# Optimization experiments

Hardware: AMD Instinct MI355X
Metric: run time of the kernel (lower is better)

## Reference

```python
import jax, jax.numpy as jnp
import numpy as np

DIM = 384
H = 6
D = DIM // H
MLP = 4 * DIM
SCALE = D ** -0.5
LN_EPS = 1e-5


def _ln(x, w, b):
    m = jnp.mean(x, axis=-1, keepdims=True)
    v = jnp.mean((x - m) ** 2, axis=-1, keepdims=True)
    return (x - m) * jax.lax.rsqrt(v + LN_EPS) * w + b


def setup_inputs() -> dict:
    key = jax.random.key(0)
    ks = jax.random.split(key, 8)
    B, N = 8, 1024
    x = jax.random.normal(ks[0], (B, N, DIM), dtype=jnp.float32)
    # torch nn.Linear weights are [out, in]
    qkv_w = jax.random.normal(ks[1], (3 * DIM, DIM), dtype=jnp.float32) * (DIM ** -0.5)
    proj_w = jax.random.normal(ks[2], (DIM, DIM), dtype=jnp.float32) * (DIM ** -0.5)
    proj_b = jnp.zeros((DIM,), jnp.float32)
    # L2Q params, 'quadratic' init
    alpha = jnp.full((H, 1, 1), 0.125, jnp.float32)
    beta = jnp.full((H, 1, 1), 0.5, jnp.float32)
    gamma = jnp.zeros((H, 1, 1), jnp.float32)
    ln1_w = jnp.ones((DIM,), jnp.float32)
    ln1_b = jnp.zeros((DIM,), jnp.float32)
    ln2_w = jnp.ones((DIM,), jnp.float32)
    ln2_b = jnp.zeros((DIM,), jnp.float32)
    w1 = jax.random.normal(ks[3], (MLP, DIM), dtype=jnp.float32) * (DIM ** -0.5)
    b1 = jnp.zeros((MLP,), jnp.float32)
    w2 = jax.random.normal(ks[4], (DIM, MLP), dtype=jnp.float32) * (MLP ** -0.5)
    b2 = jnp.zeros((DIM,), jnp.float32)
    return {"x": x, "qkv_w": qkv_w, "proj_w": proj_w, "proj_b": proj_b,
            "alpha": alpha, "beta": beta, "gamma": gamma,
            "ln1_w": ln1_w, "ln1_b": ln1_b, "ln2_w": ln2_w, "ln2_b": ln2_b,
            "w1": w1, "b1": b1, "w2": w2, "b2": b2}


def reference(x, qkv_w, proj_w, proj_b, alpha, beta, gamma,
              ln1_w, ln1_b, ln2_w, ln2_b, w1, b1, w2, b2):
    B, N, C = x.shape
    # --- L2Q attention on LN(x) ---
    h = _ln(x, ln1_w, ln1_b)
    qkv = (h @ qkv_w.T).reshape(B, N, 3, H, D)
    q = qkv[:, :, 0].transpose(0, 2, 1, 3)  # [B,H,N,D]
    k = qkv[:, :, 1].transpose(0, 2, 1, 3)
    v = qkv[:, :, 2].transpose(0, 2, 1, 3)
    logits = jnp.einsum('bhnd,bhmd->bhnm', q, k) * SCALE
    attn = jax.nn.relu(alpha * logits ** 2 + beta * logits + gamma)
    attn = attn / (jnp.sum(attn, axis=-1, keepdims=True) + 1e-6)
    out = jnp.einsum('bhnm,bhmd->bhnd', attn, v)
    out = out.transpose(0, 2, 1, 3).reshape(B, N, C)
    x = x + out @ proj_w.T + proj_b
    # --- MLP on LN(x), exact GELU (torch default) ---
    h2 = _ln(x, ln2_w, ln2_b)
    m = jax.nn.gelu(h2 @ w1.T + b1, approximate=False)
    x = x + m @ w2.T + b2
    return x
```

## Files before the change

kernel.cpp:

```cpp
#include <hip/hip_runtime.h>
#include <hip/hip_bf16.h>
#include <math.h>

#define DIMC 384
#define NH 6
#define HD 64
#define MLPD 1536
#define BS 8
#define SEQ 1024
#define T_TOK (BS*SEQ)
#define TC ((size_t)T_TOK*DIMC)
#define QK_SCALE 0.125f

typedef __bf16 bf16;
typedef bf16 bf16x4 __attribute__((ext_vector_type(4)));
typedef bf16 bf16x8 __attribute__((ext_vector_type(8)));
typedef float floatx4 __attribute__((ext_vector_type(4)));

__device__ __forceinline__ void async_cp16(const void* gsrc, void* ldst) {
    __builtin_amdgcn_global_load_lds(
        (const __attribute__((address_space(1))) unsigned int*)gsrc,
        (__attribute__((address_space(3))) unsigned int*)ldst,
        16, 0, 0);
}

__global__ __launch_bounds__(256)
void cvt_all(const float* __restrict__ s0, const float* __restrict__ s1,
             const float* __restrict__ s2, const float* __restrict__ s3,
             bf16* __restrict__ dst) {
    int i = blockIdx.x * 256 + threadIdx.x;
    const int n0 = 110592, n1 = 36864, n2 = 147456;
    const float4* src; int j;
    if (i < n0)           { src = (const float4*)s0; j = i; }
    else if (i < n0+n1)   { src = (const float4*)s1; j = i - n0; }
    else if (i < n0+n1+n2){ src = (const float4*)s2; j = i - n0 - n1; }
    else                  { src = (const float4*)s3; j = i - n0 - n1 - n2; }
    float4 v = src[j];
    bf16x4 o; o[0] = (bf16)v.x; o[1] = (bf16)v.y; o[2] = (bf16)v.z; o[3] = (bf16)v.w;
    ((bf16x4*)dst)[i] = o;
}

__global__ __launch_bounds__(256)
void ln_kernel(const float* __restrict__ x, const float* __restrict__ w,
               const float* __restrict__ b, bf16* __restrict__ out) {
    int row = blockIdx.x * 4 + (threadIdx.x >> 6);
    int t = threadIdx.x & 63;
    const float* xr = x + (size_t)row * DIMC;
    float vals[6];
    float s = 0.f;
    #pragma unroll
    for (int i = 0; i < 6; i++) { vals[i] = xr[t + i*64]; s += vals[i]; }
    #pragma unroll
    for (int m = 32; m; m >>= 1) s += __shfl_xor(s, m);
    float mean = s * (1.0f / DIMC);
    float sq = 0.f;
    #pragma unroll
    for (int i = 0; i < 6; i++) { float d = vals[i] - mean; sq += d * d; }
    #pragma unroll
    for (int m = 32; m; m >>= 1) sq += __shfl_xor(sq, m);
    float rstd = rsqrtf(sq * (1.0f / DIMC) + 1e-5f);
    bf16* orow = out + (size_t)row * DIMC;
    #pragma unroll
    for (int i = 0; i < 6; i++) {
        int c = t + i*64;
        orow[c] = (bf16)((vals[i] - mean) * rstd * w[c] + b[c]);
    }
}

__global__ __launch_bounds__(256)
void ln2_fused(const float* __restrict__ x, const bf16* __restrict__ p0,
               const bf16* __restrict__ p1, const float* __restrict__ pb,
               const float* __restrict__ w, const float* __restrict__ b,
               float* __restrict__ x1, bf16* __restrict__ h) {
    int row = blockIdx.x * 4 + (threadIdx.x >> 6);
    int t = threadIdx.x & 63;
    size_t base = (size_t)row * DIMC;
    float vals[6];
    float s = 0.f;
    #pragma unroll
    for (int i = 0; i < 6; i++) {
        int c = t + i*64;
        float v = x[base + c] + (float)p0[base + c] + (float)p1[base + c] + pb[c];
        vals[i] = v; s += v;
    }
    #pragma unroll
    for (int m = 32; m; m >>= 1) s += __shfl_xor(s, m);
    float mean = s * (1.0f / DIMC);
    float sq = 0.f;
    #pragma unroll
    for (int i = 0; i < 6; i++) { float d = vals[i] - mean; sq += d * d; }
    #pragma unroll
    for (int m = 32; m; m >>= 1) sq += __shfl_xor(sq, m);
    float rstd = rsqrtf(sq * (1.0f / DIMC) + 1e-5f);
    #pragma unroll
    for (int i = 0; i < 6; i++) {
        int c = t + i*64;
        x1[base + c] = vals[i];
        h[base + c] = (bf16)((vals[i] - mean) * rstd * w[c] + b[c]);
    }
}

__global__ __launch_bounds__(256)
void reduce4(float* __restrict__ xo, const bf16* __restrict__ p0, const bf16* __restrict__ p1,
             const bf16* __restrict__ p2, const bf16* __restrict__ p3,
             const float* __restrict__ b2) {
    int i = blockIdx.x * 256 + threadIdx.x;
    float4 v = ((const float4*)xo)[i];
    int c = (i % 96) * 4;
    float4 bb = *(const float4*)(b2 + c);
    bf16x4 a0 = ((const bf16x4*)p0)[i], a1 = ((const bf16x4*)p1)[i];
    bf16x4 a2 = ((const bf16x4*)p2)[i], a3 = ((const bf16x4*)p3)[i];
    v.x += bb.x + (float)a0[0] + (float)a1[0] + (float)a2[0] + (float)a3[0];
    v.y += bb.y + (float)a0[1] + (float)a1[1] + (float)a2[1] + (float)a3[1];
    v.z += bb.z + (float)a0[2] + (float)a1[2] + (float)a2[2] + (float)a3[2];
    v.w += bb.w + (float)a0[3] + (float)a1[3] + (float)a2[3] + (float)a3[3];
    ((float4*)xo)[i] = v;
}

enum { EPI_NONE = 0, EPI_QKV = 1, EPI_GELU = 3 };

template<int EPI, int K, int KS, typename OutT>
__global__ __launch_bounds__(256)
void gemm_bt(const bf16* __restrict__ A, const bf16* __restrict__ W,
             const float* __restrict__ bias, OutT* out, int M, int N) {
    __shared__ __align__(16) bf16 Ash[128*32];
    __shared__ __align__(16) bf16 Bsh[128*32];
    constexpr int KB = K / KS;
    int tid = threadIdx.x;
    int lane = tid & 63, w = tid >> 6;
    int quad = lane >> 4, l16 = lane & 15;
    int rbase = blockIdx.y * 128 + (w >> 1) * 64;
    int cbase = blockIdx.x * 128 + (w & 1) * 64;
    int kbase = blockIdx.z * KB;
    int c1 = w * 64 + lane;
    int c2 = c1 + 256;
    const bf16* Ag1 = A + (size_t)(blockIdx.y*128 + (c1 >> 2)) * K + kbase + (c1 & 3) * 8;
    const bf16* Ag2 = A + (size_t)(blockIdx.y*128 + (c2 >> 2)) * K + kbase + (c2 & 3) * 8;
    const bf16* Wg1 = W + (size_t)(blockIdx.x*128 + (c1 >> 2)) * K + kbase + (c1 & 3) * 8;
    const bf16* Wg2 = W + (size_t)(blockIdx.x*128 + (c2 >> 2)) * K + kbase + (c2 & 3) * 8;
    bf16* As1 = Ash + c1 * 8;  bf16* As2 = Ash + c2 * 8;
    bf16* Bs1 = Bsh + c1 * 8;  bf16* Bs2 = Bsh + c2 * 8;

    int arow = (w >> 1) * 64;
    int brow = (w & 1) * 64;
    floatx4 acc[4][4] = {};
    #pragma unroll
    for (int kk = 0; kk < KB / 32; kk++) {
        __syncthreads();
        async_cp16(Ag1 + kk*32, As1);
        async_cp16(Ag2 + kk*32, As2);
        async_cp16(Wg1 + kk*32, Bs1);
        async_cp16(Wg2 + kk*32, Bs2);
        __syncthreads();
        bf16x8 a[4], bfr[4];
        #pragma unroll
        for (int tm = 0; tm < 4; tm++)
            a[tm] = *(const bf16x8*)&Ash[(arow + tm*16 + l16) * 32 + quad*8];
        #pragma unroll
        for (int tn = 0; tn < 4; tn++)
            bfr[tn] = *(const bf16x8*)&Bsh[(brow + tn*16 + l16) * 32 + quad*8];
        #pragma unroll
        for (int tm = 0; tm < 4; tm++)
            #pragma unroll
            for (int tn = 0; tn < 4; tn++)
                acc[tm][tn] = __builtin_amdgcn_mfma_f32_16x16x32_bf16(a[tm], bfr[tn], acc[tm][tn], 0, 0, 0);
    }

    #pragma unroll
    for (int tm = 0; tm < 4; tm++)
        #pragma unroll
        for (int tn = 0; tn < 4; tn++) {
            if constexpr (EPI == EPI_QKV) {
                int colb = cbase + tn*16 + l16;
                int which = colb / 384;
                int rowb = rbase + tm*16 + quad*4;
                int bb = rowb >> 10;
                if (which == 2) {
                    int rem = colb - 768;
                    int hh = rem >> 6, d = rem & 63;
                    int n = rowb & 1023;
                    bf16x4 pk;
                    #pragma unroll
                    for (int r = 0; r < 4; r++) pk[r] = (bf16)acc[tm][tn][r];
                    *(bf16x4*)((bf16*)out + 2*TC + (((size_t)(bb*NH + hh) * HD + d) << 10) + n) = pk;
                } else {
                    int rem = colb - which*384;
                    int hh = rem >> 6, d = rem & 63;
                    #pragma unroll
                    for (int r = 0; r < 4; r++) {
                        int n = (rowb & 1023) + r;
                        ((bf16*)out)[(size_t)which*TC + (((size_t)(bb*NH + hh) * SEQ + n) << 6) + d]
                            = (bf16)acc[tm][tn][r];
                    }
                }
            } else if constexpr (EPI == EPI_NONE) {
                OutT* ob = out + (size_t)blockIdx.z * M * N;
                #pragma unroll
                for (int r = 0; r < 4; r++) {
                    int row = rbase + tm*16 + quad*4 + r;
                    int col = cbase + tn*16 + l16;
                    ob[(size_t)row * N + col] = (OutT)acc[tm][tn][r];
                }
            } else {
                #pragma unroll
                for (int r = 0; r < 4; r++) {
                    int row = rbase + tm*16 + quad*4 + r;
                    int col = cbase + tn*16 + l16;
                    float v = acc[tm][tn][r] + bias[col];
                    v = 0.5f * v * (1.0f + erff(v * 0.70710678118f));
                    out[(size_t)row * N + col] = (OutT)v;
                }
            }
        }
}

__global__ __launch_bounds__(256)
void attn_kernel(const bf16* __restrict__ q, const bf16* __restrict__ k,
                 const bf16* __restrict__ vt, const float* __restrict__ alpha,
                 const float* __restrict__ beta, const float* __restrict__ gamma,
                 bf16* __restrict__ attn_out) {
    __shared__ __align__(16) char smem[36864];
    bf16  (*Psh)[72] = (bf16(*)[72])smem;
    float (*RedA)[68] = (float(*)[68])smem;
    float (*RedB)[68] = RedA + 64;

    int L = blockIdx.x;
    int xcd = L & 7, slot = L >> 3;
    int qt = slot & 15;
    int bh = xcd + ((slot >> 4) << 3);
    int bb = bh / NH, h = bh % NH;
    int q0 = qt * 64;
    int tid = threadIdx.x;
    int w = tid >> 6, lane = tid & 63, quad = lane >> 4, l16 = lane & 15;
    float av = alpha[h] * (QK_SCALE * QK_SCALE), bv = beta[h] * QK_SCALE, gv = gamma[h];
    const bf16* qb  = q  + (size_t)bh * SEQ * HD;
    const bf16* kb  = k  + (size_t)bh * SEQ * HD;
    const bf16* vtb = vt + (size_t)bh * HD * SEQ;

    bf16x8 qa[4][2];
    #pragma unroll
    for (int tm = 0; tm < 4; tm++)
        #pragma unroll
        for (int ks = 0; ks < 2; ks++)
            qa[tm][ks] = *(const bf16x8*)(qb + (size_t)(q0 + tm*16 + l16) * HD + ks*32 + quad*8);

    bf16x8 vone;
    #pragma unroll
    for (int j = 0; j < 8; j++) vone[j] = (bf16)1.0f;

    floatx4 o[4][4] = {};
    floatx4 rsacc[4] = {};
    int prow = w * 64;
    int rd_sw = ((l16 >> 2) & 3) << 3;
    int kt_base = w * 4;

    bf16x8 kf[2][4], kn[2][4], vf[2][4];
    #pragma unroll
    for (int ks = 0; ks < 2; ks++)
        #pragma unroll
        for (int tn = 0; tn < 4; tn++)
            kf[ks][tn] = *(const bf16x8*)(kb + (size_t)(kt_base*64 + tn*16 + l16) * HD + ks*32 + quad*8);

    #pragma unroll
    for (int t = 0; t < 4; t++) {
        int kb0 = (kt_base + t) * 64;
        if (t < 3) {
            int nb0 = kb0 + 64;
            #pragma unroll
            for (int ks = 0; ks < 2; ks++)
                #pragma unroll
                for (int tn = 0; tn < 4; tn++)
                    kn[ks][tn] = *(const bf16x8*)(kb + (size_t)(nb0 + tn*16 + l16) * HD + ks*32 + quad*8);
        }
        #pragma unroll
        for (int ks = 0; ks < 2; ks++)
            #pragma unroll
            for (int tn = 0; tn < 4; tn++)
                vf[ks][tn] = *(const bf16x8*)(vtb + (size_t)(tn*16 + l16) * SEQ + kb0 + ks*32 + quad*8);
        #pragma unroll
        for (int tm = 0; tm < 4; tm++) {
            floatx4 s[4] = {};
            #pragma unroll
            for (int ks = 0; ks < 2; ks++)
                #pragma unroll
                for (int tn = 0; tn < 4; tn++)
                    s[tn] = __builtin_amdgcn_mfma_f32_16x16x32_bf16(qa[tm][ks], kf[ks][tn], s[tn], 0, 0, 0);
            #pragma unroll
            for (int tn = 0; tn < 4; tn++)
                #pragma unroll
                for (int r = 0; r < 4; r++) {
                    float xx = s[tn][r];
                    float p = fmaxf((av*xx + bv)*xx + gv, 0.f);
                    int row = tm*16 + quad*4 + r;
                    int col = (tn*16 + l16) ^ (quad << 3);
                    Psh[prow + row][col] = (bf16)p;
                }
        }
        #pragma unroll
        for (int ks = 0; ks < 2; ks++) {
            bf16x8 pf[4];
            #pragma unroll
            for (int tm = 0; tm < 4; tm++)
                pf[tm] = *(const bf16x8*)&Psh[prow + tm*16 + l16][(ks*32 + quad*8) ^ rd_sw];
            #pragma unroll
            for (int tm = 0; tm < 4; tm++)
                rsacc[tm] = __builtin_amdgcn_mfma_f32_16x16x32_bf16(pf[tm], vone, rsacc[tm], 0, 0, 0);
            #pragma unroll
            for (int tm = 0; tm < 4; tm++)
                #pragma unroll
                for (int tn = 0; tn < 4; tn++)
                    o[tm][tn] = __builtin_amdgcn_mfma_f32_16x16x32_bf16(pf[tm], vf[ks][tn], o[tm][tn], 0, 0, 0);
        }
        if (t < 3) {
            #pragma unroll
            for (int ks = 0; ks < 2; ks++)
                #pragma unroll
                for (int tn = 0; tn < 4; tn++)
                    kf[ks][tn] = kn[ks][tn];
        }
    }

    __syncthreads();
    if (w & 1) {
        float (*R)[68] = (w == 1) ? RedA : RedB;
        #pragma unroll
        for (int tm = 0; tm < 4; tm++) {
            #pragma unroll
            for (int tn = 0; tn < 4; tn++)
                #pragma unroll
                for (int r = 0; r < 4; r++)
                    R[tm*16 + quad*4 + r][tn*16 + l16] = o[tm][tn][r];
            if (l16 == 0)
                #pragma unroll
                for (int r = 0; r < 4; r++)
                    R[tm*16 + quad*4 + r][64] = rsacc[tm][r];
        }
    }
    __syncthreads();
    if (!(w & 1)) {
        float (*R)[68] = (w == 0) ? RedA : RedB;
        #pragma unroll
        for (int tm = 0; tm < 4; tm++) {
            #pragma unroll
            for (int tn = 0; tn < 4; tn++)
                #pragma unroll
                for (int r = 0; r < 4; r++)
                    o[tm][tn][r] += R[tm*16 + quad*4 + r][tn*16 + l16];
            #pragma unroll
            for (int r = 0; r < 4; r++)
                rsacc[tm][r] += R[tm*16 + quad*4 + r][64];
        }
    }
    __syncthreads();
    if (w == 2) {
        #pragma unroll
        for (int tm = 0; tm < 2; tm++) {
            #pragma unroll
            for (int tn = 0; tn < 4; tn++)
                #pragma unroll
                for (int r = 0; r < 4; r++)
                    RedA[tm*16 + quad*4 + r][tn*16 + l16] = o[tm][tn][r];
            if (l16 == 0)
                #pragma unroll
                for (int r = 0; r < 4; r++)
                    RedA[tm*16 + quad*4 + r][64] = rsacc[tm][r];
        }
    } else if (w == 0) {
        #pragma unroll
        for (int tm = 2; tm < 4; tm++) {
            #pragma unroll
            for (int tn = 0; tn < 4; tn++)
                #pragma unroll
                for (int r = 0; r < 4; r++)
                    RedA[tm*16 + quad*4 + r][tn*16 + l16] = o[tm][tn][r];
            if (l16 == 0)
                #pragma unroll
                for (int r = 0; r < 4; r++)
                    RedA[tm*16 + quad*4 + r][64] = rsacc[tm][r];
        }
    }
    __syncthreads();
    if (w == 0) {
        #pragma unroll
        for (int tm = 0; tm < 2; tm++) {
            #pragma unroll
            for (int r = 0; r < 4; r++)
                rsacc[tm][r] += RedA[tm*16 + quad*4 + r][64];
            #pragma unroll
            for (int tn = 0; tn < 4; tn++)
                #pragma unroll
                for (int r = 0; r < 4; r++) {
                    float ov = o[tm][tn][r] + RedA[tm*16 + quad*4 + r][tn*16 + l16];
                    int n = q0 + tm*16 + quad*4 + r;
                    attn_out[((size_t)(bb*SEQ + n)) * DIMC + h*HD + tn*16 + l16] =
                        (bf16)(ov / (rsacc[tm][r] + 1e-6f));
                }
        }
    } else if (w == 2) {
        #pragma unroll
        for (int tm = 2; tm < 4; tm++) {
            #pragma unroll
            for (int r = 0; r < 4; r++)
                rsacc[tm][r] += RedA[tm*16 + quad*4 + r][64];
            #pragma unroll
            for (int tn = 0; tn < 4; tn++)
                #pragma unroll
                for (int r = 0; r < 4; r++) {
                    float ov = o[tm][tn][r] + RedA[tm*16 + quad*4 + r][tn*16 + l16];
                    int n = q0 + tm*16 + quad*4 + r;
                    attn_out[((size_t)(bb*SEQ + n)) * DIMC + h*HD + tn*16 + l16] =
                        (bf16)(ov / (rsacc[tm][r] + 1e-6f));
                }
        }
    }
}

extern "C" void kernel_launch(void* const* d_in, const int* in_sizes, int n_in,
                              void* d_out, int out_size, void* d_ws, size_t ws_size,
                              hipStream_t stream) {
    const float* x      = (const float*)d_in[0];
    const float* qkv_w  = (const float*)d_in[1];
    const float* proj_w = (const float*)d_in[2];
    const float* proj_b = (const float*)d_in[3];
    const float* alpha  = (const float*)d_in[4];
    const float* beta   = (const float*)d_in[5];
    const float* gamma  = (const float*)d_in[6];
    const float* ln1_w  = (const float*)d_in[7];
    const float* ln1_b  = (const float*)d_in[8];
    const float* ln2_w  = (const float*)d_in[9];
    const float* ln2_b  = (const float*)d_in[10];
    const float* w1     = (const float*)d_in[11];
    const float* b1     = (const float*)d_in[12];
    const float* w2     = (const float*)d_in[13];
    const float* b2     = (const float*)d_in[14];
    float* out = (float*)d_out;

    char* base = (char*)d_ws;
    bf16* wq_bf = (bf16*)base;
    bf16* wp_bf = wq_bf + 442368;
    bf16* w1_bf = wq_bf + 589824;
    bf16* w2_bf = wq_bf + 1179648;
    bf16* h      = (bf16*)(base + 3538944);
    bf16* qkv    = (bf16*)(base + 9830400);
    bf16* attn_o = (bf16*)(base + 28704768);
    bf16* m      = qkv;
    bf16* Pp     = (bf16*)(base + 34996224);
    bf16* Pm     = (bf16*)(base + 34996224);

    cvt_all<<<1728, 256, 0, stream>>>(qkv_w, proj_w, w1, w2, wq_bf);
    ln_kernel<<<T_TOK/4, 256, 0, stream>>>(x, ln1_w, ln1_b, h);
    gemm_bt<EPI_QKV, 384, 1, bf16><<<dim3(9, 64, 1), 256, 0, stream>>>(
        h, wq_bf, nullptr, qkv, T_TOK, 1152);
    attn_kernel<<<768, 256, 0, stream>>>(
        qkv, qkv + TC, qkv + 2*TC, alpha, beta, gamma, attn_o);
    gemm_bt<EPI_NONE, 384, 2, bf16><<<dim3(3, 64, 2), 256, 0, stream>>>(
        attn_o, wp_bf, nullptr, Pp, T_TOK, DIMC);
    ln2_fused<<<T_TOK/4, 256, 0, stream>>>(x, Pp, Pp + TC, proj_b, ln2_w, ln2_b, out, h);
    gemm_bt<EPI_GELU, 384, 1, bf16><<<dim3(12, 64, 1), 256, 0, stream>>>(
        h, w1_bf, b1, m, T_TOK, MLPD);
    gemm_bt<EPI_NONE, 1536, 4, bf16><<<dim3(3, 64, 4), 256, 0, stream>>>(
        m, w2_bf, nullptr, Pm, T_TOK, DIMC);
    reduce4<<<TC/4/256, 256, 0, stream>>>(out, Pm, Pm + TC, Pm + 2*TC, Pm + 3*TC, b2);
}
```

Baseline: 233.2 us.

## Halve attention query tile to 32 rows and double grid for occupancy

The attention kernel now processes 32 query rows per block instead of 64. The grid doubles to 1536 blocks, shared memory halves, and launch bounds request 4 blocks per CU. The K prefetch double-buffer is dropped: the next K tile is loaded straight into kf after QK^T, and V loads move after the P write, cutting register pressure. This trades per-block K/V reuse (each K/V tile is reloaded by twice as many blocks) for more waves in flight to hide latency.

```diff
diff --git a/kernel.cpp b/kernel.cpp
--- a/kernel.cpp
+++ b/kernel.cpp
@@ -214,22 +214,22 @@
         }
 }
 
-__global__ __launch_bounds__(256)
+__global__ __launch_bounds__(256, 4)
 void attn_kernel(const bf16* __restrict__ q, const bf16* __restrict__ k,
                  const bf16* __restrict__ vt, const float* __restrict__ alpha,
                  const float* __restrict__ beta, const float* __restrict__ gamma,
                  bf16* __restrict__ attn_out) {
-    __shared__ __align__(16) char smem[36864];
+    __shared__ __align__(16) char smem[18432];
     bf16  (*Psh)[72] = (bf16(*)[72])smem;
     float (*RedA)[68] = (float(*)[68])smem;
-    float (*RedB)[68] = RedA + 64;
+    float (*RedB)[68] = RedA + 32;
 
     int L = blockIdx.x;
     int xcd = L & 7, slot = L >> 3;
-    int qt = slot & 15;
-    int bh = xcd + ((slot >> 4) << 3);
+    int qt = slot & 31;
+    int bh = xcd + ((slot >> 5) << 3);
     int bb = bh / NH, h = bh % NH;
-    int q0 = qt * 64;
+    int q0 = qt * 32;
     int tid = threadIdx.x;
     int w = tid >> 6, lane = tid & 63, quad = lane >> 4, l16 = lane & 15;
     float av = alpha[h] * (QK_SCALE * QK_SCALE), bv = beta[h] * QK_SCALE, gv = gamma[h];
@@ -237,9 +237,9 @@
     const bf16* kb  = k  + (size_t)bh * SEQ * HD;
     const bf16* vtb = vt + (size_t)bh * HD * SEQ;
 
-    bf16x8 qa[4][2];
-    #pragma unroll
-    for (int tm = 0; tm < 4; tm++)
+    bf16x8 qa[2][2];
+    #pragma unroll
+    for (int tm = 0; tm < 2; tm++)
         #pragma unroll
         for (int ks = 0; ks < 2; ks++)
             qa[tm][ks] = *(const bf16x8*)(qb + (size_t)(q0 + tm*16 + l16) * HD + ks*32 + quad*8);
@@ -248,13 +248,13 @@
     #pragma unroll
     for (int j = 0; j < 8; j++) vone[j] = (bf16)1.0f;
 
-    floatx4 o[4][4] = {};
-    floatx4 rsacc[4] = {};
-    int prow = w * 64;
+    floatx4 o[2][4] = {};
+    floatx4 rsacc[2] = {};
+    int prow = w * 32;
     int rd_sw = ((l16 >> 2) & 3) << 3;
     int kt_base = w * 4;
 
-    bf16x8 kf[2][4], kn[2][4], vf[2][4];
+    bf16x8 kf[2][4], vf[2][4];
     #pragma unroll
     for (int ks = 0; ks < 2; ks++)
         #pragma unroll
@@ -264,21 +264,8 @@
     #pragma unroll
     for (int t = 0; t < 4; t++) {
         int kb0 = (kt_base + t) * 64;
-        if (t < 3) {
-            int nb0 = kb0 + 64;
-            #pragma unroll
-            for (int ks = 0; ks < 2; ks++)
-                #pragma unroll
-                for (int tn = 0; tn < 4; tn++)
-                    kn[ks][tn] = *(const bf16x8*)(kb + (size_t)(nb0 + tn*16 + l16) * HD + ks*32 + quad*8);
-        }
-        #pragma unroll
-        for (int ks = 0; ks < 2; ks++)
-            #pragma unroll
-            for (int tn = 0; tn < 4; tn++)
-                vf[ks][tn] = *(const bf16x8*)(vtb + (size_t)(tn*16 + l16) * SEQ + kb0 + ks*32 + quad*8);
-        #pragma unroll
-        for (int tm = 0; tm < 4; tm++) {
+        #pragma unroll
+        for (int tm = 0; tm < 2; tm++) {
             floatx4 s[4] = {};
             #pragma unroll
             for (int ks = 0; ks < 2; ks++)
@@ -296,27 +283,33 @@
                     Psh[prow + row][col] = (bf16)p;
                 }
         }
+        if (t < 3) {
+            int nb0 = kb0 + 64;
+            #pragma unroll
+            for (int ks = 0; ks < 2; ks++)
+                #pragma unroll
+                for (int tn = 0; tn < 4; tn++)
+                    kf[ks][tn] = *(const bf16x8*)(kb + (size_t)(nb0 + tn*16 + l16) * HD + ks*32 + quad*8);
+        }
+        #pragma unroll
+        for (int ks = 0; ks < 2; ks++)
+            #pragma unroll
+            for (int tn = 0; tn < 4; tn++)
+                vf[ks][tn] = *(const bf16x8*)(vtb + (size_t)(tn*16 + l16) * SEQ + kb0 + ks*32 + quad*8);
         #pragma unroll
         for (int ks = 0; ks < 2; ks++) {
-            bf16x8 pf[4];
-            #pragma unroll
-            for (int tm = 0; tm < 4; tm++)
+            bf16x8 pf[2];
+            #pragma unroll
+            for (int tm = 0; tm < 2; tm++)
                 pf[tm] = *(const bf16x8*)&Psh[prow + tm*16 + l16][(ks*32 + quad*8) ^ rd_sw];
             #pragma unroll
-            for (int tm = 0; tm < 4; tm++)
+            for (int tm = 0; tm < 2; tm++)
                 rsacc[tm] = __builtin_amdgcn_mfma_f32_16x16x32_bf16(pf[tm], vone, rsacc[tm], 0, 0, 0);
             #pragma unroll
-            for (int tm = 0; tm < 4; tm++)
+            for (int tm = 0; tm < 2; tm++)
                 #pragma unroll
                 for (int tn = 0; tn < 4; tn++)
                     o[tm][tn] = __builtin_amdgcn_mfma_f32_16x16x32_bf16(pf[tm], vf[ks][tn], o[tm][tn], 0, 0, 0);
-        }
-        if (t < 3) {
-            #pragma unroll
-            for (int ks = 0; ks < 2; ks++)
-                #pragma unroll
-                for (int tn = 0; tn < 4; tn++)
-                    kf[ks][tn] = kn[ks][tn];
         }
     }
 
@@ -324,7 +317,7 @@
     if (w & 1) {
         float (*R)[68] = (w == 1) ? RedA : RedB;
         #pragma unroll
-        for (int tm = 0; tm < 4; tm++) {
+        for (int tm = 0; tm < 2; tm++) {
             #pragma unroll
             for (int tn = 0; tn < 4; tn++)
                 #pragma unroll
@@ -340,7 +333,7 @@
     if (!(w & 1)) {
         float (*R)[68] = (w == 0) ? RedA : RedB;
         #pragma unroll
-        for (int tm = 0; tm < 4; tm++) {
+        for (int tm = 0; tm < 2; tm++) {
             #pragma unroll
             for (int tn = 0; tn < 4; tn++)
                 #pragma unroll
@@ -354,64 +347,52 @@
     __syncthreads();
     if (w == 2) {
         #pragma unroll
-        for (int tm = 0; tm < 2; tm++) {
-            #pragma unroll
-            for (int tn = 0; tn < 4; tn++)
-                #pragma unroll
-                for (int r = 0; r < 4; r++)
-                    RedA[tm*16 + quad*4 + r][tn*16 + l16] = o[tm][tn][r];
-            if (l16 == 0)
-                #pragma unroll
-                for (int r = 0; r < 4; r++)
-                    RedA[tm*16 + quad*4 + r][64] = rsacc[tm][r];
-        }
+        for (int tn = 0; tn < 4; tn++)
+            #pragma unroll
+            for (int r = 0; r < 4; r++)
+                RedA[quad*4 + r][tn*16 + l16] = o[0][tn][r];
+        if (l16 == 0)
+            #pragma unroll
+            for (int r = 0; r < 4; r++)
+                RedA[quad*4 + r][64] = rsacc[0][r];
     } else if (w == 0) {
         #pragma unroll
-        for (int tm = 2; tm < 4; tm++) {
-            #pragma unroll
-            for (int tn = 0; tn < 4; tn++)
-                #pragma unroll
-                for (int r = 0; r < 4; r++)
-                    RedA[tm*16 + quad*4 + r][tn*16 + l16] = o[tm][tn][r];
-            if (l16 == 0)
-                #pragma unroll
-                for (int r = 0; r < 4; r++)
-                    RedA[tm*16 + quad*4 + r][64] = rsacc[tm][r];
-        }
+        for (int tn = 0; tn < 4; tn++)
+            #pragma unroll
+            for (int r = 0; r < 4; r++)
+                RedA[16 + quad*4 + r][tn*16 + l16] = o[1][tn][r];
+        if (l16 == 0)
+            #pragma unroll
+            for (int r = 0; r < 4; r++)
+                RedA[16 + quad*4 + r][64] = rsacc[1][r];
     }
     __syncthreads();
     if (w == 0) {
         #pragma unroll
-        for (int tm = 0; tm < 2; tm++) {
-            #pragma unroll
-            for (int r = 0; r < 4; r++)
-                rsacc[tm][r] += RedA[tm*16 + quad*4 + r][64];
-            #pragma unroll
-            for (int tn = 0; tn < 4; tn++)
-                #pragma unroll
-                for (int r = 0; r < 4; r++) {
-                    float ov = o[tm][tn][r] + RedA[tm*16 + quad*4 + r][tn*16 + l16];
-                    int n = q0 + tm*16 + quad*4 + r;
-                    attn_out[((size_t)(bb*SEQ + n)) * DIMC + h*HD + tn*16 + l16] =
-                        (bf16)(ov / (rsacc[tm][r] + 1e-6f));
-                }
-        }
+        for (int r = 0; r < 4; r++)
+            rsacc[0][r] += RedA[quad*4 + r][64];
+        #pragma unroll
+        for (int tn = 0; tn < 4; tn++)
+            #pragma unroll
+            for (int r = 0; r < 4; r++) {
+                float ov = o[0][tn][r] + RedA[quad*4 + r][tn*16 + l16];
+                int n = q0 + quad*4 + r;
+                attn_out[((size_t)(bb*SEQ + n)) * DIMC + h*HD + tn*16 + l16] =
+                    (bf16)(ov / (rsacc[0][r] + 1e-6f));
+            }
     } else if (w == 2) {
         #pragma unroll
-        for (int tm = 2; tm < 4; tm++) {
-            #pragma unroll
-            for (int r = 0; r < 4; r++)
-                rsacc[tm][r] += RedA[tm*16 + quad*4 + r][64];
-            #pragma unroll
-            for (int tn = 0; tn < 4; tn++)
-                #pragma unroll
-                for (int r = 0; r < 4; r++) {
-                    float ov = o[tm][tn][r] + RedA[tm*16 + quad*4 + r][tn*16 + l16];
-                    int n = q0 + tm*16 + quad*4 + r;
-                    attn_out[((size_t)(bb*SEQ + n)) * DIMC + h*HD + tn*16 + l16] =
-                        (bf16)(ov / (rsacc[tm][r] + 1e-6f));
-                }
-        }
+        for (int r = 0; r < 4; r++)
+            rsacc[1][r] += RedA[16 + quad*4 + r][64];
+        #pragma unroll
+        for (int tn = 0; tn < 4; tn++)
+            #pragma unroll
+            for (int r = 0; r < 4; r++) {
+                float ov = o[1][tn][r] + RedA[16 + quad*4 + r][tn*16 + l16];
+                int n = q0 + 16 + quad*4 + r;
+                attn_out[((size_t)(bb*SEQ + n)) * DIMC + h*HD + tn*16 + l16] =
+                    (bf16)(ov / (rsacc[1][r] + 1e-6f));
+            }
     }
 }
 
@@ -451,7 +432,7 @@
     ln_kernel<<<T_TOK/4, 256, 0, stream>>>(x, ln1_w, ln1_b, h);
     gemm_bt<EPI_QKV, 384, 1, bf16><<<dim3(9, 64, 1), 256, 0, stream>>>(
         h, wq_bf, nullptr, qkv, T_TOK, 1152);
-    attn_kernel<<<768, 256, 0, stream>>>(
+    attn_kernel<<<1536, 256, 0, stream>>>(
         qkv, qkv + TC, qkv + 2*TC, alpha, beta, gamma, attn_o);
     gemm_bt<EPI_NONE, 384, 2, bf16><<<dim3(3, 64, 2), 256, 0, stream>>>(
         attn_o, wp_bf, nullptr, Pp, T_TOK, DIMC);
```

Result: slower. 240.0 us (+2.9%).
